# Kernel optimization log

Measured on AMD Instinct MI355X. Metric: run time of the kernel, lower is better.

The kernel has to match this reference:

```python
import jax, jax.numpy as jnp
import numpy as np
from jax import lax

WINDOW_SIZE = 11
SIGMA = 1.5
DATA_RANGE = 1.0


def _gaussian_window(channels):
    coords = jnp.arange(WINDOW_SIZE, dtype=jnp.float32) - WINDOW_SIZE // 2
    g = jnp.exp(-coords ** 2 / (2.0 * SIGMA ** 2))
    g = g / g.sum()
    w2d = jnp.outer(g, g)
    w2d = w2d / w2d.sum()
    # depthwise kernel: (C, 1, K, K) in OIHW with feature_group_count=C
    return jnp.broadcast_to(w2d, (channels, 1, WINDOW_SIZE, WINDOW_SIZE))


def _dwconv(x, window, channels):
    pad = WINDOW_SIZE // 2
    return lax.conv_general_dilated(
        x, window,
        window_strides=(1, 1),
        padding=[(pad, pad), (pad, pad)],
        dimension_numbers=('NCHW', 'OIHW', 'NCHW'),
        feature_group_count=channels,
    )


def setup_inputs() -> dict:
    key = jax.random.key(0)
    k1, k2 = jax.random.split(key)
    B, C, H, W = 16, 3, 512, 512
    x = jax.random.uniform(k1, (B, C, H, W), dtype=jnp.float32)
    y = jax.random.uniform(k2, (B, C, H, W), dtype=jnp.float32)
    return {"x": x, "y": y}


def reference(x, y):
    channels = x.shape[1]
    window = _gaussian_window(channels)
    mu_x = _dwconv(x, window, channels)
    mu_y = _dwconv(y, window, channels)
    mu_x2 = mu_x * mu_x
    mu_y2 = mu_y * mu_y
    mu_xy = mu_x * mu_y
    sigma_x2 = _dwconv(x * x, window, channels) - mu_x2
    sigma_y2 = _dwconv(y * y, window, channels) - mu_y2
    sigma_xy = _dwconv(x * y, window, channels) - mu_xy
    c1 = (0.01 * DATA_RANGE) ** 2
    c2 = (0.03 * DATA_RANGE) ** 2
    ssim_map = (2 * mu_xy + c1) * (2 * sigma_xy + c2) / (
        (mu_x2 + mu_y2 + c1) * (sigma_x2 + sigma_y2 + c2) + 1e-08)
    per_image = ssim_map.mean(axis=(1, 2, 3))
    return 1.0 - per_image.mean()
```

## Files before the change

### kernel.cpp

```cpp
#include <hip/hip_runtime.h>
#include <math.h>


#define IMG_W 512
#define IMG_H 512
#define PLANES 48
#define TYS 128
#define RAD 5
#define NT 128
#define NWAVES (PLANES * 32 * (IMG_H / TYS))
#define NBLKS (NWAVES / 2)
#define NCH 9
#define NCV 8
#define CSTR 40
#define PSTR (16 * CSTR)
#define WSTR (4 * PSTR)
#define NUMREC (IMG_W * IMG_H * 4)
#define CHSTEP (16 * IMG_W * 4)
#define INVW  0.26601181f
#define GC2   0.32059890f

typedef _Float16 h2 __attribute__((ext_vector_type(2)));
typedef _Float16 h4 __attribute__((ext_vector_type(4)));
typedef _Float16 h8 __attribute__((ext_vector_type(8)));
typedef float f32x4 __attribute__((ext_vector_type(4)));
typedef int i32x4 __attribute__((ext_vector_type(4)));

__device__ f32x4 buf_ld_x4(i32x4 srsrc, int voffset, int soffset, int aux)
    __asm("llvm.amdgcn.raw.buffer.load.v4f32");

__device__ __forceinline__ i32x4 make_srd(const float* p) {
    union { i32x4 v; struct { const float* p; unsigned rng; unsigned cfg; } s; } u;
    u.s.p = p; u.s.rng = NUMREC; u.s.cfg = 0x00020000u;
    return u.v;
}

__device__ __forceinline__ float exp2_fast(float a) {
#if __has_builtin(__builtin_amdgcn_exp2f)
    return __builtin_amdgcn_exp2f(a);
#else
    return exp2f(a);
#endif
}

__device__ __forceinline__ float wbandf(int idx) {
    const float fd = (float)(idx - 5);
    const float g = exp2_fast(-(fd * fd) * GC2) * INVW;
    return ((unsigned)idx <= 10u) ? g : 0.f;
}

__device__ __forceinline__ h2 pkrtz(float a, float b) {
    auto t = __builtin_amdgcn_cvt_pkrtz(a, b);
    h2 r;
    __builtin_memcpy(&r, &t, sizeof(r));
    return r;
}

__device__ __forceinline__ h4 pack4(f32x4 a) {
    const h2 lo = pkrtz(a[0], a[1]), hi = pkrtz(a[2], a[3]);
    h4 v;
    v[0] = lo.x; v[1] = lo.y; v[2] = hi.x; v[3] = hi.y;
    return v;
}

__device__ __forceinline__ void hconv_chunk(
    f32x4 xa, f32x4 xb, f32x4 ya, f32x4 yb, h8 whB,
    _Float16* wp)
{
    const f32x4 zz = {0.f, 0.f, 0.f, 0.f};
    const h2 xh0 = pkrtz(xa[0], xa[1]), xh1 = pkrtz(xa[2], xa[3]);
    const h2 xh2 = pkrtz(xb[0], xb[1]), xh3 = pkrtz(xb[2], xb[3]);
    const h2 yh0 = pkrtz(ya[0], ya[1]), yh1 = pkrtz(ya[2], ya[3]);
    const h2 yh2 = pkrtz(yb[0], yb[1]), yh3 = pkrtz(yb[2], yb[3]);
    const h2 s0 = xh0 + yh0, s1 = xh1 + yh1, s2 = xh2 + yh2, s3 = xh3 + yh3;
    const h2 d0 = xh0 - yh0, d1 = xh1 - yh1, d2 = xh2 - yh2, d3 = xh3 - yh3;
    h8 sA, dA;
    sA[0] = s0.x; sA[1] = s0.y; sA[2] = s1.x; sA[3] = s1.y;
    sA[4] = s2.x; sA[5] = s2.y; sA[6] = s3.x; sA[7] = s3.y;
    dA[0] = d0.x; dA[1] = d0.y; dA[2] = d1.x; dA[3] = d1.y;
    dA[4] = d2.x; dA[5] = d2.y; dA[6] = d3.x; dA[7] = d3.y;
    const h8 s2A = sA * sA;
    const h8 d2A = dA * dA;
    const f32x4 hS  = __builtin_amdgcn_mfma_f32_16x16x32_f16(sA,  whB, zz, 0, 0, 0);
    const f32x4 hD  = __builtin_amdgcn_mfma_f32_16x16x32_f16(dA,  whB, zz, 0, 0, 0);
    const f32x4 hS2 = __builtin_amdgcn_mfma_f32_16x16x32_f16(s2A, whB, zz, 0, 0, 0);
    const f32x4 hD2 = __builtin_amdgcn_mfma_f32_16x16x32_f16(d2A, whB, zz, 0, 0, 0);
    *(h4*)(wp + 0 * PSTR) = pack4(hS);
    *(h4*)(wp + 1 * PSTR) = pack4(hD);
    *(h4*)(wp + 2 * PSTR) = pack4(hS2);
    *(h4*)(wp + 3 * PSTR) = pack4(hD2);
}

__device__ __forceinline__ float mapsum(f32x4 aS, f32x4 aD, f32x4 aS2, f32x4 aD2,
                                        float cv)
{
    float local = 0.f;
    #pragma unroll
    for (int r = 0; r < 4; ++r) {
        const float mS = aS[r]  * cv, mD = aD[r]  * cv;
        const float eS = aS2[r] * cv, eD = aD2[r] * cv;
        const float ms2 = mS * mS, md2 = mD * mD;
        const float Pm = 0.5f * (ms2 - md2);
        const float Qm = 0.5f * (ms2 + md2);
        const float Pe = 0.5f * (eS - eD);
        const float Qe = 0.5f * (eS + eD);
        const float c1 = 1e-4f, c2 = 9e-4f;
        const float num = (Pm + c1) * (Pe - Pm + c2);
        const float den = (Qm + c1) * (Qe - Qm + c2) + 1e-8f;
        local += num * __builtin_amdgcn_rcpf(den);
    }
    return local;
}

#define MFMA16(A, B, C) __builtin_amdgcn_mfma_f32_16x16x32_f16((A), (B), (C), 0, 0, 0)

__global__ __launch_bounds__(NT, 7) void ssim_tile_kernel(
    const float* __restrict__ x, const float* __restrict__ y,
    float* __restrict__ partials)
{
    __shared__ __align__(16) _Float16 Ht[2 * WSTR];

    const int tid = threadIdx.x;
    const int l = tid & 63, wid = tid >> 6;
    const int q = l >> 4, fc = l & 15;
    const int ql = q & 1, qh = q >> 1;

    const int gid = blockIdx.x * 2 + wid;
    const int plane = gid >> 7;
    const int rem = gid & 127;
    const int R0 = (rem >> 5) * TYS;
    const int C0 = (rem & 31) * 16;

    const i32x4 srdx = make_srd(x + (size_t)plane * IMG_H * IMG_W);
    const i32x4 srdy = make_srd(y + (size_t)plane * IMG_H * IMG_W);
    const int gcol = C0 - 8 + 8 * q;
    int voff = ((unsigned)gcol < (unsigned)IMG_W)
             ? (((R0 - RAD + fc) << 11) + (gcol << 2)) : 0x60000000;

    f32x4 LXA[2], LXB[2], LYA[2], LYB[2];
    #pragma unroll
    for (int cpl = 0; cpl < 2; ++cpl) {
        LXA[cpl] = buf_ld_x4(srdx, voff, 0, 0);
        LXB[cpl] = buf_ld_x4(srdx, voff, 16, 0);
        LYA[cpl] = buf_ld_x4(srdy, voff, 0, 0);
        LYB[cpl] = buf_ld_x4(srdy, voff, 16, 0);
        voff += CHSTEP;
    }

    float s2w = 0.f;
    #pragma unroll
    for (int k = 0; k <= 10; ++k) s2w += (float)(_Float16)wbandf(k);
    const float cv = 1.f / (s2w * s2w);

    h8 whB, wvA;
    #pragma unroll
    for (int e = 0; e < 8; ++e) {
        whB[e] = (_Float16)wbandf(8 * q + e - fc - 3);
        wvA[e] = (_Float16)wbandf(8 * q + e - fc);
    }

    _Float16* const Hw = Ht + wid * WSTR;
    _Float16* const hwr = Hw + fc * CSTR + 4 * q;
    const _Float16* const rbase = Hw + fc * CSTR + 8 * ql;

    const f32x4 zz = {0.f, 0.f, 0.f, 0.f};
    float local = 0.f;

    #pragma unroll
    for (int c = 0; c < NCH; ++c) {
        if (c >= 2) {
            const _Float16* rp = rbase + (((c + qh) & 1) << 4);
            const h8 B0 = *(const h8*)(rp + 0 * PSTR);
            const h8 B1 = *(const h8*)(rp + 1 * PSTR);
            const h8 B2 = *(const h8*)(rp + 2 * PSTR);
            const h8 B3 = *(const h8*)(rp + 3 * PSTR);
            const f32x4 aS  = MFMA16(wvA, B0, zz);
            const f32x4 aD  = MFMA16(wvA, B1, zz);
            const f32x4 aS2 = MFMA16(wvA, B2, zz);
            const f32x4 aD2 = MFMA16(wvA, B3, zz);
            local += mapsum(aS, aD, aS2, aD2, cv);
        }
        hconv_chunk(LXA[c & 1], LXB[c & 1], LYA[c & 1], LYB[c & 1],
                    whB, hwr + ((c & 1) << 4));
        if (c + 2 < NCH) {
            LXA[c & 1] = buf_ld_x4(srdx, voff, 0, 0);
            LXB[c & 1] = buf_ld_x4(srdx, voff, 16, 0);
            LYA[c & 1] = buf_ld_x4(srdy, voff, 0, 0);
            LYB[c & 1] = buf_ld_x4(srdy, voff, 16, 0);
            voff += CHSTEP;
        }
    }

    {
        const _Float16* rp = rbase + ((((NCH - 2) + qh) & 1) << 4);
        const h8 B0 = *(const h8*)(rp + 0 * PSTR);
        const h8 B1 = *(const h8*)(rp + 1 * PSTR);
        const h8 B2 = *(const h8*)(rp + 2 * PSTR);
        const h8 B3 = *(const h8*)(rp + 3 * PSTR);
        const f32x4 aS  = MFMA16(wvA, B0, zz);
        const f32x4 aD  = MFMA16(wvA, B1, zz);
        const f32x4 aS2 = MFMA16(wvA, B2, zz);
        const f32x4 aD2 = MFMA16(wvA, B3, zz);
        local += mapsum(aS, aD, aS2, aD2, cv);
    }

    #pragma unroll
    for (int off = 32; off > 0; off >>= 1)
        local += __shfl_down(local, off, 64);
    if (l == 0) partials[gid] = local;
}

__global__ __launch_bounds__(256) void ssim_finalize_kernel(
    const float* __restrict__ partials, float* __restrict__ out)
{
    const int tid = threadIdx.x;
    double s = 0.0;
    #pragma unroll 4
    for (int i = tid; i < NWAVES; i += 256) s += (double)partials[i];
    #pragma unroll
    for (int off = 32; off > 0; off >>= 1)
        s += __shfl_down(s, off, 64);
    __shared__ double ws_[256 / 64];
    const int lane = tid & 63, wv = tid >> 6;
    if (lane == 0) ws_[wv] = s;
    __syncthreads();
    if (tid == 0) {
        const double t = ws_[0] + ws_[1] + ws_[2] + ws_[3];
        const double n = (double)PLANES * IMG_H * IMG_W;
        out[0] = (float)(1.0 - t / n);
    }
}

extern "C" void kernel_launch(void* const* d_in, const int* in_sizes, int n_in,
                              void* d_out, int out_size, void* d_ws, size_t ws_size,
                              hipStream_t stream)
{
    const float* x = (const float*)d_in[0];
    const float* y = (const float*)d_in[1];
    float* out = (float*)d_out;
    float* partials = (float*)d_ws;

    dim3 grid(NBLKS, 1, 1);
    ssim_tile_kernel<<<grid, NT, 0, stream>>>(x, y, partials);
    ssim_finalize_kernel<<<1, 256, 0, stream>>>(partials, out);
}
```

Before: 144.9 us.

## Deepen global-load pipeline to three stages with inline-asm buffer loads and 4-wave blocks

```diff
diff --git a/kernel.cpp b/kernel.cpp
--- a/kernel.cpp
+++ b/kernel.cpp
@@ -5,13 +5,15 @@
 #define IMG_W 512
 #define IMG_H 512
 #define PLANES 48
+#define TX 64
 #define TYS 128
 #define RAD 5
-#define NT 128
-#define NWAVES (PLANES * 32 * (IMG_H / TYS))
-#define NBLKS (NWAVES / 2)
+#define NT 256
+#define GDX (IMG_W / TX)
+#define GDY (IMG_H / TYS)
+#define NBLK (GDX * GDY * PLANES)
+#define NWAVES (NBLK * 4)
 #define NCH 9
-#define NCV 8
 #define CSTR 40
 #define PSTR (16 * CSTR)
 #define WSTR (4 * PSTR)
@@ -26,13 +28,16 @@
 typedef float f32x4 __attribute__((ext_vector_type(4)));
 typedef int i32x4 __attribute__((ext_vector_type(4)));
 
-__device__ f32x4 buf_ld_x4(i32x4 srsrc, int voffset, int soffset, int aux)
-    __asm("llvm.amdgcn.raw.buffer.load.v4f32");
-
 __device__ __forceinline__ i32x4 make_srd(const float* p) {
     union { i32x4 v; struct { const float* p; unsigned rng; unsigned cfg; } s; } u;
     u.s.p = p; u.s.rng = NUMREC; u.s.cfg = 0x00020000u;
     return u.v;
+}
+
+template<int N>
+__device__ __forceinline__ void vwait() {
+    asm volatile("s_waitcnt vmcnt(%0)" :: "n"(N) : "memory");
+    __builtin_amdgcn_sched_barrier(0);
 }
 
 __device__ __forceinline__ float exp2_fast(float a) {
@@ -114,38 +119,54 @@
 
 #define MFMA16(A, B, C) __builtin_amdgcn_mfma_f32_16x16x32_f16((A), (B), (C), 0, 0, 0)
 
-__global__ __launch_bounds__(NT, 7) void ssim_tile_kernel(
+#define ISSUE(slot) do {                                                      \
+    asm volatile("buffer_load_dwordx4 %0, %1, %2, 0 offen"                    \
+                 : "=v"(LXA[slot]) : "v"(voff), "s"(srdx));                   \
+    asm volatile("buffer_load_dwordx4 %0, %1, %2, 0 offen offset:16"          \
+                 : "=v"(LXB[slot]) : "v"(voff), "s"(srdx));                   \
+    asm volatile("buffer_load_dwordx4 %0, %1, %2, 0 offen"                    \
+                 : "=v"(LYA[slot]) : "v"(voff), "s"(srdy));                   \
+    asm volatile("buffer_load_dwordx4 %0, %1, %2, 0 offen offset:16"          \
+                 : "=v"(LYB[slot]) : "v"(voff), "s"(srdy));                   \
+    voff += CHSTEP;                                                           \
+} while (0)
+
+#define VCONV(C) do {                                                         \
+    const _Float16* rp = rbase + ((((C) + qh) & 1) << 4);                     \
+    const h8 B0 = *(const h8*)(rp + 0 * PSTR);           \
+    const h8 B1 = *(const h8*)(rp + 1 * PSTR);                                \
+    const h8 B2 = *(const h8*)(rp + 2 * PSTR);                                \
+    const h8 B3 = *(const h8*)(rp + 3 * PSTR);                                \
+    const f32x4 aS  = MFMA16(wvA, B0, zz);                                    \
+    const f32x4 aD  = MFMA16(wvA, B1, zz);                                    \
+    const f32x4 aS2 = MFMA16(wvA, B2, zz);                                    \
+    const f32x4 aD2 = MFMA16(wvA, B3, zz);                                    \
+    local += mapsum(aS, aD, aS2, aD2, cv);                                    \
+} while (0)
+
+__global__ __launch_bounds__(NT, 4) void ssim_tile_kernel(
     const float* __restrict__ x, const float* __restrict__ y,
     float* __restrict__ partials)
 {
-    __shared__ __align__(16) _Float16 Ht[2 * WSTR];
+    __shared__ __align__(16) _Float16 Ht[4 * WSTR];
 
     const int tid = threadIdx.x;
     const int l = tid & 63, wid = tid >> 6;
     const int q = l >> 4, fc = l & 15;
     const int ql = q & 1, qh = q >> 1;
 
-    const int gid = blockIdx.x * 2 + wid;
-    const int plane = gid >> 7;
-    const int rem = gid & 127;
-    const int R0 = (rem >> 5) * TYS;
-    const int C0 = (rem & 31) * 16;
-
+    const int plane = blockIdx.z;
     const i32x4 srdx = make_srd(x + (size_t)plane * IMG_H * IMG_W);
     const i32x4 srdy = make_srd(y + (size_t)plane * IMG_H * IMG_W);
-    const int gcol = C0 - 8 + 8 * q;
+    const int C0 = blockIdx.x * TX;
+    const int R0 = blockIdx.y * TYS;
+    const int c0 = 16 * wid;
+    const int gcol = C0 + c0 - 8 + 8 * q;
     int voff = ((unsigned)gcol < (unsigned)IMG_W)
              ? (((R0 - RAD + fc) << 11) + (gcol << 2)) : 0x60000000;
 
-    f32x4 LXA[2], LXB[2], LYA[2], LYB[2];
-    #pragma unroll
-    for (int cpl = 0; cpl < 2; ++cpl) {
-        LXA[cpl] = buf_ld_x4(srdx, voff, 0, 0);
-        LXB[cpl] = buf_ld_x4(srdx, voff, 16, 0);
-        LYA[cpl] = buf_ld_x4(srdy, voff, 0, 0);
-        LYB[cpl] = buf_ld_x4(srdy, voff, 16, 0);
-        voff += CHSTEP;
-    }
+    f32x4 LXA[3], LXB[3], LYA[3], LYB[3];
+    ISSUE(0); ISSUE(1); ISSUE(2);
 
     float s2w = 0.f;
     #pragma unroll
@@ -168,45 +189,21 @@
 
     #pragma unroll
     for (int c = 0; c < NCH; ++c) {
-        if (c >= 2) {
-            const _Float16* rp = rbase + (((c + qh) & 1) << 4);
-            const h8 B0 = *(const h8*)(rp + 0 * PSTR);
-            const h8 B1 = *(const h8*)(rp + 1 * PSTR);
-            const h8 B2 = *(const h8*)(rp + 2 * PSTR);
-            const h8 B3 = *(const h8*)(rp + 3 * PSTR);
-            const f32x4 aS  = MFMA16(wvA, B0, zz);
-            const f32x4 aD  = MFMA16(wvA, B1, zz);
-            const f32x4 aS2 = MFMA16(wvA, B2, zz);
-            const f32x4 aD2 = MFMA16(wvA, B3, zz);
-            local += mapsum(aS, aD, aS2, aD2, cv);
-        }
-        hconv_chunk(LXA[c & 1], LXB[c & 1], LYA[c & 1], LYB[c & 1],
+        if (c >= 2) VCONV(c);
+        if (c <= 6) vwait<8>();
+        else if (c == 7) vwait<4>();
+        else vwait<0>();
+        hconv_chunk(LXA[c % 3], LXB[c % 3], LYA[c % 3], LYB[c % 3],
                     whB, hwr + ((c & 1) << 4));
-        if (c + 2 < NCH) {
-            LXA[c & 1] = buf_ld_x4(srdx, voff, 0, 0);
-            LXB[c & 1] = buf_ld_x4(srdx, voff, 16, 0);
-            LYA[c & 1] = buf_ld_x4(srdy, voff, 0, 0);
-            LYB[c & 1] = buf_ld_x4(srdy, voff, 16, 0);
-            voff += CHSTEP;
-        }
-    }
-
-    {
-        const _Float16* rp = rbase + ((((NCH - 2) + qh) & 1) << 4);
-        const h8 B0 = *(const h8*)(rp + 0 * PSTR);
-        const h8 B1 = *(const h8*)(rp + 1 * PSTR);
-        const h8 B2 = *(const h8*)(rp + 2 * PSTR);
-        const h8 B3 = *(const h8*)(rp + 3 * PSTR);
-        const f32x4 aS  = MFMA16(wvA, B0, zz);
-        const f32x4 aD  = MFMA16(wvA, B1, zz);
-        const f32x4 aS2 = MFMA16(wvA, B2, zz);
-        const f32x4 aD2 = MFMA16(wvA, B3, zz);
-        local += mapsum(aS, aD, aS2, aD2, cv);
-    }
+        if (c + 3 < NCH) ISSUE(c % 3);
+    }
+
+    VCONV(9);
 
     #pragma unroll
     for (int off = 32; off > 0; off >>= 1)
         local += __shfl_down(local, off, 64);
+    const int gid = (blockIdx.x + GDX * (blockIdx.y + GDY * blockIdx.z)) * 4 + wid;
     if (l == 0) partials[gid] = local;
 }
 
@@ -240,7 +237,7 @@
     float* out = (float*)d_out;
     float* partials = (float*)d_ws;
 
-    dim3 grid(NBLKS, 1, 1);
+    dim3 grid(GDX, GDY, PLANES);
     ssim_tile_kernel<<<grid, NT, 0, stream>>>(x, y, partials);
     ssim_finalize_kernel<<<1, 256, 0, stream>>>(partials, out);
 }
```

Result: faster. 131.2 us (-9.5%).

## Replace LDS transpose with ds_bpermute and split vertical MFMA across chunks

Applied to the files above, without the earlier changes.

```diff
diff --git a/kernel.cpp b/kernel.cpp
--- a/kernel.cpp
+++ b/kernel.cpp
@@ -5,23 +5,21 @@
 #define IMG_W 512
 #define IMG_H 512
 #define PLANES 48
+#define TX 64
 #define TYS 128
 #define RAD 5
-#define NT 128
-#define NWAVES (PLANES * 32 * (IMG_H / TYS))
-#define NBLKS (NWAVES / 2)
+#define NT 256
+#define GDX (IMG_W / TX)
+#define GDY (IMG_H / TYS)
+#define NBLK (GDX * GDY * PLANES)
+#define NWAVES (NBLK * 4)
 #define NCH 9
-#define NCV 8
-#define CSTR 40
-#define PSTR (16 * CSTR)
-#define WSTR (4 * PSTR)
 #define NUMREC (IMG_W * IMG_H * 4)
 #define CHSTEP (16 * IMG_W * 4)
 #define INVW  0.26601181f
 #define GC2   0.32059890f
 
 typedef _Float16 h2 __attribute__((ext_vector_type(2)));
-typedef _Float16 h4 __attribute__((ext_vector_type(4)));
 typedef _Float16 h8 __attribute__((ext_vector_type(8)));
 typedef float f32x4 __attribute__((ext_vector_type(4)));
 typedef int i32x4 __attribute__((ext_vector_type(4)));
@@ -56,39 +54,20 @@
     return r;
 }
 
-__device__ __forceinline__ h4 pack4(f32x4 a) {
+__device__ __forceinline__ void packdw(f32x4 a, int& d0, int& d1) {
     const h2 lo = pkrtz(a[0], a[1]), hi = pkrtz(a[2], a[3]);
-    h4 v;
-    v[0] = lo.x; v[1] = lo.y; v[2] = hi.x; v[3] = hi.y;
-    return v;
-}
-
-__device__ __forceinline__ void hconv_chunk(
-    f32x4 xa, f32x4 xb, f32x4 ya, f32x4 yb, h8 whB,
-    _Float16* wp)
-{
-    const f32x4 zz = {0.f, 0.f, 0.f, 0.f};
-    const h2 xh0 = pkrtz(xa[0], xa[1]), xh1 = pkrtz(xa[2], xa[3]);
-    const h2 xh2 = pkrtz(xb[0], xb[1]), xh3 = pkrtz(xb[2], xb[3]);
-    const h2 yh0 = pkrtz(ya[0], ya[1]), yh1 = pkrtz(ya[2], ya[3]);
-    const h2 yh2 = pkrtz(yb[0], yb[1]), yh3 = pkrtz(yb[2], yb[3]);
-    const h2 s0 = xh0 + yh0, s1 = xh1 + yh1, s2 = xh2 + yh2, s3 = xh3 + yh3;
-    const h2 d0 = xh0 - yh0, d1 = xh1 - yh1, d2 = xh2 - yh2, d3 = xh3 - yh3;
-    h8 sA, dA;
-    sA[0] = s0.x; sA[1] = s0.y; sA[2] = s1.x; sA[3] = s1.y;
-    sA[4] = s2.x; sA[5] = s2.y; sA[6] = s3.x; sA[7] = s3.y;
-    dA[0] = d0.x; dA[1] = d0.y; dA[2] = d1.x; dA[3] = d1.y;
-    dA[4] = d2.x; dA[5] = d2.y; dA[6] = d3.x; dA[7] = d3.y;
-    const h8 s2A = sA * sA;
-    const h8 d2A = dA * dA;
-    const f32x4 hS  = __builtin_amdgcn_mfma_f32_16x16x32_f16(sA,  whB, zz, 0, 0, 0);
-    const f32x4 hD  = __builtin_amdgcn_mfma_f32_16x16x32_f16(dA,  whB, zz, 0, 0, 0);
-    const f32x4 hS2 = __builtin_amdgcn_mfma_f32_16x16x32_f16(s2A, whB, zz, 0, 0, 0);
-    const f32x4 hD2 = __builtin_amdgcn_mfma_f32_16x16x32_f16(d2A, whB, zz, 0, 0, 0);
-    *(h4*)(wp + 0 * PSTR) = pack4(hS);
-    *(h4*)(wp + 1 * PSTR) = pack4(hD);
-    *(h4*)(wp + 2 * PSTR) = pack4(hS2);
-    *(h4*)(wp + 3 * PSTR) = pack4(hD2);
+    __builtin_memcpy(&d0, &lo, 4);
+    __builtin_memcpy(&d1, &hi, 4);
+}
+
+__device__ __forceinline__ h8 bperm_frag(int idxA, int idxB, int pd0, int pd1) {
+    const int b0 = __builtin_amdgcn_ds_bpermute(idxA, pd0);
+    const int b1 = __builtin_amdgcn_ds_bpermute(idxA, pd1);
+    const int b2 = __builtin_amdgcn_ds_bpermute(idxB, pd0);
+    const int b3 = __builtin_amdgcn_ds_bpermute(idxB, pd1);
+    union { i32x4 i; h8 h; } u;
+    u.i = i32x4{b0, b1, b2, b3};
+    return u.h;
 }
 
 __device__ __forceinline__ float mapsum(f32x4 aS, f32x4 aD, f32x4 aS2, f32x4 aD2,
@@ -114,28 +93,26 @@
 
 #define MFMA16(A, B, C) __builtin_amdgcn_mfma_f32_16x16x32_f16((A), (B), (C), 0, 0, 0)
 
-__global__ __launch_bounds__(NT, 7) void ssim_tile_kernel(
+__global__ __launch_bounds__(NT, 4) void ssim_tile_kernel(
     const float* __restrict__ x, const float* __restrict__ y,
     float* __restrict__ partials)
 {
-    __shared__ __align__(16) _Float16 Ht[2 * WSTR];
-
     const int tid = threadIdx.x;
     const int l = tid & 63, wid = tid >> 6;
     const int q = l >> 4, fc = l & 15;
-    const int ql = q & 1, qh = q >> 1;
-
-    const int gid = blockIdx.x * 2 + wid;
-    const int plane = gid >> 7;
-    const int rem = gid & 127;
-    const int R0 = (rem >> 5) * TYS;
-    const int C0 = (rem & 31) * 16;
-
+
+    const int plane = blockIdx.z;
     const i32x4 srdx = make_srd(x + (size_t)plane * IMG_H * IMG_W);
     const i32x4 srdy = make_srd(y + (size_t)plane * IMG_H * IMG_W);
-    const int gcol = C0 - 8 + 8 * q;
+    const int C0 = blockIdx.x * TX;
+    const int R0 = blockIdx.y * TYS;
+    const int c0 = 16 * wid;
+    const int gcol = C0 + c0 - 8 + 8 * q;
     int voff = ((unsigned)gcol < (unsigned)IMG_W)
              ? (((R0 - RAD + fc) << 11) + (gcol << 2)) : 0x60000000;
+
+    const int idxA = ((l & 16) << 3) | ((l & 15) << 2);
+    const int idxB = idxA + 64;
 
     f32x4 LXA[2], LXB[2], LYA[2], LYB[2];
     #pragma unroll
@@ -152,36 +129,23 @@
     for (int k = 0; k <= 10; ++k) s2w += (float)(_Float16)wbandf(k);
     const float cv = 1.f / (s2w * s2w);
 
-    h8 whB, wvA;
+    h8 whB, wvA1, wvA2;
     #pragma unroll
     for (int e = 0; e < 8; ++e) {
-        whB[e] = (_Float16)wbandf(8 * q + e - fc - 3);
-        wvA[e] = (_Float16)wbandf(8 * q + e - fc);
-    }
-
-    _Float16* const Hw = Ht + wid * WSTR;
-    _Float16* const hwr = Hw + fc * CSTR + 4 * q;
-    const _Float16* const rbase = Hw + fc * CSTR + 8 * ql;
+        const int k = 8 * q + e;
+        whB[e]  = (_Float16)wbandf(k - fc - 3);
+        wvA1[e] = (_Float16)((k < 16) ? wbandf(k - fc)      : 0.f);
+        wvA2[e] = (_Float16)((k < 16) ? wbandf(k + 16 - fc) : 0.f);
+    }
 
     const f32x4 zz = {0.f, 0.f, 0.f, 0.f};
+    f32x4 acc[4];
     float local = 0.f;
 
     #pragma unroll
     for (int c = 0; c < NCH; ++c) {
-        if (c >= 2) {
-            const _Float16* rp = rbase + (((c + qh) & 1) << 4);
-            const h8 B0 = *(const h8*)(rp + 0 * PSTR);
-            const h8 B1 = *(const h8*)(rp + 1 * PSTR);
-            const h8 B2 = *(const h8*)(rp + 2 * PSTR);
-            const h8 B3 = *(const h8*)(rp + 3 * PSTR);
-            const f32x4 aS  = MFMA16(wvA, B0, zz);
-            const f32x4 aD  = MFMA16(wvA, B1, zz);
-            const f32x4 aS2 = MFMA16(wvA, B2, zz);
-            const f32x4 aD2 = MFMA16(wvA, B3, zz);
-            local += mapsum(aS, aD, aS2, aD2, cv);
-        }
-        hconv_chunk(LXA[c & 1], LXB[c & 1], LYA[c & 1], LYB[c & 1],
-                    whB, hwr + ((c & 1) << 4));
+        const f32x4 xa = LXA[c & 1], xb = LXB[c & 1];
+        const f32x4 ya = LYA[c & 1], yb = LYB[c & 1];
         if (c + 2 < NCH) {
             LXA[c & 1] = buf_ld_x4(srdx, voff, 0, 0);
             LXB[c & 1] = buf_ld_x4(srdx, voff, 16, 0);
@@ -189,24 +153,50 @@
             LYB[c & 1] = buf_ld_x4(srdy, voff, 16, 0);
             voff += CHSTEP;
         }
-    }
-
-    {
-        const _Float16* rp = rbase + ((((NCH - 2) + qh) & 1) << 4);
-        const h8 B0 = *(const h8*)(rp + 0 * PSTR);
-        const h8 B1 = *(const h8*)(rp + 1 * PSTR);
-        const h8 B2 = *(const h8*)(rp + 2 * PSTR);
-        const h8 B3 = *(const h8*)(rp + 3 * PSTR);
-        const f32x4 aS  = MFMA16(wvA, B0, zz);
-        const f32x4 aD  = MFMA16(wvA, B1, zz);
-        const f32x4 aS2 = MFMA16(wvA, B2, zz);
-        const f32x4 aD2 = MFMA16(wvA, B3, zz);
-        local += mapsum(aS, aD, aS2, aD2, cv);
+        const h2 xh0 = pkrtz(xa[0], xa[1]), xh1 = pkrtz(xa[2], xa[3]);
+        const h2 xh2 = pkrtz(xb[0], xb[1]), xh3 = pkrtz(xb[2], xb[3]);
+        const h2 yh0 = pkrtz(ya[0], ya[1]), yh1 = pkrtz(ya[2], ya[3]);
+        const h2 yh2 = pkrtz(yb[0], yb[1]), yh3 = pkrtz(yb[2], yb[3]);
+        const h2 s0 = xh0 + yh0, s1 = xh1 + yh1, s2 = xh2 + yh2, s3 = xh3 + yh3;
+        const h2 d0 = xh0 - yh0, d1 = xh1 - yh1, d2 = xh2 - yh2, d3 = xh3 - yh3;
+        h8 sA, dA;
+        sA[0] = s0.x; sA[1] = s0.y; sA[2] = s1.x; sA[3] = s1.y;
+        sA[4] = s2.x; sA[5] = s2.y; sA[6] = s3.x; sA[7] = s3.y;
+        dA[0] = d0.x; dA[1] = d0.y; dA[2] = d1.x; dA[3] = d1.y;
+        dA[4] = d2.x; dA[5] = d2.y; dA[6] = d3.x; dA[7] = d3.y;
+        const h8 s2A = sA * sA;
+        const h8 d2A = dA * dA;
+        const f32x4 hS  = MFMA16(sA,  whB, zz);
+        const f32x4 hD  = MFMA16(dA,  whB, zz);
+        const f32x4 hS2 = MFMA16(s2A, whB, zz);
+        const f32x4 hD2 = MFMA16(d2A, whB, zz);
+
+        int pd0, pd1;
+        h8 B[4];
+        packdw(hS,  pd0, pd1); B[0] = bperm_frag(idxA, idxB, pd0, pd1);
+        packdw(hD,  pd0, pd1); B[1] = bperm_frag(idxA, idxB, pd0, pd1);
+        packdw(hS2, pd0, pd1); B[2] = bperm_frag(idxA, idxB, pd0, pd1);
+        packdw(hD2, pd0, pd1); B[3] = bperm_frag(idxA, idxB, pd0, pd1);
+
+        if (c >= 1) {
+            const f32x4 fS  = MFMA16(wvA2, B[0], acc[0]);
+            const f32x4 fD  = MFMA16(wvA2, B[1], acc[1]);
+            const f32x4 fS2 = MFMA16(wvA2, B[2], acc[2]);
+            const f32x4 fD2 = MFMA16(wvA2, B[3], acc[3]);
+            local += mapsum(fS, fD, fS2, fD2, cv);
+        }
+        if (c < NCH - 1) {
+            acc[0] = MFMA16(wvA1, B[0], zz);
+            acc[1] = MFMA16(wvA1, B[1], zz);
+            acc[2] = MFMA16(wvA1, B[2], zz);
+            acc[3] = MFMA16(wvA1, B[3], zz);
+        }
     }
 
     #pragma unroll
     for (int off = 32; off > 0; off >>= 1)
         local += __shfl_down(local, off, 64);
+    const int gid = (blockIdx.x + GDX * (blockIdx.y + GDY * blockIdx.z)) * 4 + wid;
     if (l == 0) partials[gid] = local;
 }
 
@@ -240,7 +230,7 @@
     float* out = (float*)d_out;
     float* partials = (float*)d_ws;
 
-    dim3 grid(NBLKS, 1, 1);
+    dim3 grid(GDX, GDY, PLANES);
     ssim_tile_kernel<<<grid, NT, 0, stream>>>(x, y, partials);
     ssim_finalize_kernel<<<1, 256, 0, stream>>>(partials, out);
 }
```

New measurement: 135.5 us. 6.5% less time.
